# Kernel tuning notes

Hardware: AMD Instinct MI355X
Metric: run time of the kernel (lower is better)

The kernel has to match this reference:

```python
import jax, jax.numpy as jnp
import numpy as np
import math

E = 512      # embed_dim
H = 8        # num_heads
HD = E // H  # head_dim
S = 2048     # seq_len
B = 4        # batch


def setup_inputs() -> dict:
    key = jax.random.key(0)
    ks = jax.random.split(key, 8)
    std = 1.0 / math.sqrt(E)
    return {
        "query": jax.random.normal(ks[0], (S, B, E), jnp.float32),
        "key": jax.random.normal(ks[1], (S, B, E), jnp.float32),
        "value": jax.random.normal(ks[2], (S, B, E), jnp.float32),
        "relative_pos_bias": jax.random.normal(ks[3], (H, S, S), jnp.float32),
        "in_proj_weight": jax.random.normal(ks[4], (3 * E, E), jnp.float32) * std,
        "in_proj_bias": jnp.zeros((3 * E,), jnp.float32),
        "out_proj_weight": jax.random.normal(ks[5], (E, E), jnp.float32) * std,
        "out_proj_bias": jnp.zeros((E,), jnp.float32),
    }


def reference(query, key, value, relative_pos_bias,
              in_proj_weight, in_proj_bias, out_proj_weight, out_proj_bias):
    # batch_first=False: inputs are (S, B, E). Self-attn style: q,k,v all projected
    # from their respective inputs with the fused in_proj (query used for q-slice, etc.)
    wq, wk, wv = jnp.split(in_proj_weight, 3, axis=0)
    bq, bk, bv = jnp.split(in_proj_bias, 3, axis=0)
    # NOTE: original applies F.linear(q, full_in_proj) then chunks, with q==query etc.
    # Here query/key/value are distinct tensors but the torch code projects qkv from
    # the SAME tensor q (the query input). Replicate that exactly:
    qkv = query @ in_proj_weight.T + in_proj_bias          # (S, B, 3E)
    q, k, v = jnp.split(qkv, 3, axis=-1)                    # each (S, B, E)
    q = q.reshape(S, B, H, HD)
    k = k.reshape(S, B, H, HD)
    v = v.reshape(S, B, H, HD)
    scale = 1.0 / math.sqrt(HD)
    # scores: (B, H, S, S)
    scores = jnp.einsum('ibhd,jbhd->bhij', q, k) * scale
    bias = jnp.clip(relative_pos_bias, -5.0, 5.0)[None]     # (1, H, S, S)
    scores = scores + bias * 0.05
    scores = jnp.clip(scores, -30.0, 30.0)
    m = jax.lax.stop_gradient(jnp.max(scores, axis=-1, keepdims=True))
    attn_weights = jax.nn.softmax(scores - m, axis=-1)       # (B, H, S, S)
    out = jnp.einsum('bhij,jbhd->ibhd', attn_weights, v)     # (S, B, H, HD)
    out = jnp.where(jnp.isnan(out), 0.0, out)
    # torch: view(B,H,S,hd).transpose(1,2).view(B,S,E) == our (S,B,H,HD)->(B,S,E)
    out = out.transpose(1, 0, 2, 3).reshape(B, S, E)
    out = jnp.clip(out, -10.0, 10.0)
    out = out @ out_proj_weight.T + out_proj_bias            # (B, S, E)
    out = jnp.where(jnp.isnan(out), 0.0, out)
    # batch_first=False: return (S, B, E)
    return out.transpose(1, 0, 2), attn_weights
```

## Files before the change

### kernel.cpp

```cpp
#include <hip/hip_runtime.h>
#include <hip/hip_bf16.h>

#define S_LEN 2048
#define BATCH 4
#define EMB   512
#define NH    8
#define HD    64
#define SB    (S_LEN*BATCH)
#define E3    (3*EMB)
#define BH    (BATCH*NH)

typedef _Float16 f16;
typedef _Float16 f16x4 __attribute__((ext_vector_type(4)));
typedef _Float16 f16x8 __attribute__((ext_vector_type(8)));
typedef float    f32x4 __attribute__((ext_vector_type(4)));

#define LDS_FENCE() do { asm volatile("s_waitcnt lgkmcnt(0)" ::: "memory"); \
                         __builtin_amdgcn_sched_barrier(0); } while (0)

__global__ __launch_bounds__(256) void k_cast(const float* __restrict__ q,
    const float* __restrict__ wi, const float* __restrict__ wo,
    f16* __restrict__ qh, f16* __restrict__ wih, f16* __restrict__ woh)
{
    const int NQ4 = (SB*EMB)/4, NW4 = (E3*EMB)/4, NO4 = (EMB*EMB)/4;
    const int total = NQ4 + NW4 + NO4;
    for (int i = blockIdx.x * 256 + threadIdx.x; i < total; i += gridDim.x * 256) {
        const float* src; f16* dst; int j;
        if (i < NQ4)            { src = q;  dst = qh;  j = i; }
        else if (i < NQ4 + NW4) { src = wi; dst = wih; j = i - NQ4; }
        else                    { src = wo; dst = woh; j = i - NQ4 - NW4; }
        f32x4 v = *(const f32x4*)(src + (size_t)j * 4);
        f16x4 h4;
        #pragma unroll
        for (int jj = 0; jj < 4; ++jj) h4[jj] = (f16)v[jj];
        *(f16x4*)(dst + (size_t)j * 4) = h4;
    }
}

__global__ __launch_bounds__(256) void k_qkv_h(const f16* __restrict__ Ah,
    const f16* __restrict__ Bw, const float* __restrict__ bin,
    f16* __restrict__ Qh, f16* __restrict__ Kh, f16* __restrict__ Vh)
{
    __shared__ f16 As[128 * 64];
    __shared__ f16 Bs[128 * 64];
    const int tid = threadIdx.x;
    const int w = tid >> 6, l = tid & 63;
    const int g = l >> 4, li = l & 15;
    const int wm = w >> 1, wn = w & 1;
    const int row0 = blockIdx.x * 128;
    const int col0 = blockIdx.y * 128;

    const int srow = tid >> 3;
    const int sch  = tid & 7;
    const f16* ga = Ah + (size_t)(row0 + srow) * EMB + sch * 8;
    const f16* gb = Bw + (size_t)(col0 + srow) * EMB + sch * 8;

    f16x8 ra[4], rb[4];
    #pragma unroll
    for (int r = 0; r < 4; ++r) {
        ra[r] = *(const f16x8*)(ga + (size_t)r * 32 * EMB);
        rb[r] = *(const f16x8*)(gb + (size_t)r * 32 * EMB);
    }

    f32x4 acc[4][4];
    const f32x4 zero = {0.f, 0.f, 0.f, 0.f};
    #pragma unroll
    for (int m = 0; m < 4; ++m)
        #pragma unroll
        for (int n = 0; n < 4; ++n) acc[m][n] = zero;

    for (int kt = 0; kt < 8; ++kt) {
        __syncthreads();
        #pragma unroll
        for (int r = 0; r < 4; ++r) {
            const int rw = srow + 32 * r;
            const int po = rw * 64 + ((sch ^ (rw & 7)) << 3);
            *(f16x8*)&As[po] = ra[r];
            *(f16x8*)&Bs[po] = rb[r];
        }
        __syncthreads();
        if (kt < 7) {
            const int kn = (kt + 1) * 64;
            #pragma unroll
            for (int r = 0; r < 4; ++r) {
                ra[r] = *(const f16x8*)(ga + kn + (size_t)r * 32 * EMB);
                rb[r] = *(const f16x8*)(gb + kn + (size_t)r * 32 * EMB);
            }
        }
        #pragma unroll
        for (int kb = 0; kb < 2; ++kb) {
            f16x8 af[4], bf[4];
            #pragma unroll
            for (int m = 0; m < 4; ++m)
                af[m] = *(const f16x8*)&As[(wm*64 + m*16 + li) * 64 +
                                           (((kb*4 + g) ^ (li & 7)) << 3)];
            #pragma unroll
            for (int n = 0; n < 4; ++n)
                bf[n] = *(const f16x8*)&Bs[(wn*64 + n*16 + li) * 64 +
                                           (((kb*4 + g) ^ (li & 7)) << 3)];
            #pragma unroll
            for (int m = 0; m < 4; ++m)
                #pragma unroll
                for (int n = 0; n < 4; ++n)
                    acc[m][n] = __builtin_amdgcn_mfma_f32_16x16x32_f16(af[m], bf[n], acc[m][n], 0, 0, 0);
        }
    }

    #pragma unroll
    for (int n = 0; n < 4; ++n) {
        const int coln  = col0 + wn*64 + n*16 + li;
        const int which = coln >> 9;
        const int h     = (coln >> 6) & 7;
        const int d     = coln & 63;
        const float bb  = bin[coln];
        f16* base = (which == 0) ? Qh : (which == 1) ? Kh : Vh;
        #pragma unroll
        for (int m = 0; m < 4; ++m) {
            const int rbase = row0 + wm*64 + m*16 + g*4;
            const int s = rbase >> 2;
            #pragma unroll
            for (int jj = 0; jj < 4; ++jj) {
                const int bh = jj * NH + h;
                base[((size_t)bh * S_LEN + s) * HD + d] = (f16)(acc[m][n][jj] + bb);
            }
        }
    }
}

__global__ __launch_bounds__(256) void k_vt(const f16* __restrict__ Vh,
                                            f16* __restrict__ Vt)
{
    __shared__ f16 T[64 * 64];
    const int tid = threadIdx.x;
    const int l = tid & 63, w = tid >> 6;
    const int bh = blockIdx.y;
    const int s0 = blockIdx.x * 64;
    const int r8 = l >> 3;
    const int ch = l & 7;

    #pragma unroll
    for (int it = 0; it < 2; ++it) {
        const int srow = it * 32 + w * 8 + r8;
        f16x8 v = *(const f16x8*)&Vh[((size_t)bh * S_LEN + s0 + srow) * HD + ch * 8];
        #pragma unroll
        for (int i = 0; i < 8; ++i) {
            const int d = ch * 8 + i;
            T[d * 64 + (((srow >> 3) ^ (d & 7)) << 3) + (srow & 7)] = v[i];
        }
    }
    __syncthreads();
    #pragma unroll
    for (int it = 0; it < 2; ++it) {
        const int d = it * 32 + w * 8 + r8;
        f16x8 v = *(const f16x8*)&T[d * 64 + ((ch ^ (d & 7)) << 3)];
        *(f16x8*)&Vt[((size_t)bh * HD + d) * S_LEN + s0 + ch * 8] = v;
    }
}

__global__ __launch_bounds__(256, 4) void k_attn(
    const f16* __restrict__ Qh, const f16* __restrict__ Kh, const f16* __restrict__ Vt,
    const float* __restrict__ rpb, float* __restrict__ att, f16* __restrict__ ctxh)
{
    __shared__ f16   KT[64*64];
    __shared__ f16   VTs[64*64];
    __shared__ float SBm[4][16*64];
    __shared__ f16   PBm[4][16*64];

    const int tid = threadIdx.x;
    const int w  = tid >> 6, l = tid & 63;
    const int g  = l >> 4, li = l & 15;
    const int l8 = l >> 3, l7 = l & 7;
    const int bx = blockIdx.x;
    const int b  = bx & 3;
    const int rt = (bx >> 2) & 31;
    const int h  = bx >> 7;
    const int bh = b * NH + h;
    const int r0 = rt * 64 + w * 16;

    const f16* qbase = Qh + ((size_t)bh * S_LEN + r0 + li) * HD;
    const f16x8 bq0 = *(const f16x8*)(qbase + g * 8);
    const f16x8 bq1 = *(const f16x8*)(qbase + 32 + g * 8);

    const int sr0 = w * 16 + l8;
    const int sr1 = sr0 + 8;
    const int scl = (l7 ^ l8) * 8;
    const f16* kg0 = Kh + ((size_t)bh * S_LEN + sr0) * HD + scl;
    const f16* kg1 = Kh + ((size_t)bh * S_LEN + sr1) * HD + scl;
    const f16* vg0 = Vt + ((size_t)bh * HD + sr0) * S_LEN + scl;
    const f16* vg1 = Vt + ((size_t)bh * HD + sr1) * S_LEN + scl;
    const int stw0 = (w * 2 + 0) * 512 + l * 8;
    const int stw1 = (w * 2 + 1) * 512 + l * 8;

    const int fK0 = li * 64 + ((g ^ (li & 7)) << 3);
    const int fK1 = li * 64 + (((g + 4) ^ (li & 7)) << 3);

    float* SBw = &SBm[w][0];
    f16*   PBw = &PBm[w][0];
    const int sbr = l8 * 64 + ((l7 ^ l8) << 2);

    const float* bias0 = rpb + ((size_t)h * S_LEN + r0 + l8) * S_LEN + l7 * 4;
    const float* bias1 = bias0 + (size_t)8 * S_LEN;
    float* att0 = att + ((size_t)bh * S_LEN + r0 + l8) * S_LEN + l7 * 4;
    float* att1 = att0 + (size_t)8 * S_LEN;

    const f32x4 zero = {0.f, 0.f, 0.f, 0.f};

    float ls0 = 0.f, ls1 = 0.f;
    f16x8 tk0 = *(const f16x8*)kg0;
    f16x8 tk1 = *(const f16x8*)kg1;
    for (int t = 0; t < 32; ++t) {
        __syncthreads();
        *(f16x8*)&KT[stw0] = tk0;
        *(f16x8*)&KT[stw1] = tk1;
        __syncthreads();
        const int tn1 = (t < 31) ? t + 1 : 31;
        tk0 = *(const f16x8*)(kg0 + (size_t)tn1 * 4096);
        tk1 = *(const f16x8*)(kg1 + (size_t)tn1 * 4096);
        #pragma unroll
        for (int half = 0; half < 2; ++half) {
            #pragma unroll
            for (int n2 = 0; n2 < 2; ++n2) {
                const int n = half * 2 + n2;
                f16x8 a0 = *(const f16x8*)&KT[n * 1024 + fK0];
                f16x8 a1 = *(const f16x8*)&KT[n * 1024 + fK1];
                f32x4 st = __builtin_amdgcn_mfma_f32_16x16x32_f16(a0, bq0, zero, 0, 0, 0);
                st = __builtin_amdgcn_mfma_f32_16x16x32_f16(a1, bq1, st, 0, 0, 0);
                *(f32x4*)&SBw[li * 64 + ((((n * 4) + g) ^ (li & 7)) << 2)] = st;
            }
            LDS_FENCE();
            #pragma unroll
            for (int i = 0; i < 2; ++i) {
                f32x4 sc = *(const f32x4*)&SBw[sbr + i * 512 + half * 32];
                f32x4 bz = *(const f32x4*)((i ? bias1 : bias0) + t * 64 + half * 32);
                float acc = 0.f;
                #pragma unroll
                for (int jj = 0; jj < 4; ++jj) {
                    float bc = fminf(fmaxf(bz[jj], -5.f), 5.f) * 0.05f;
                    float v  = sc[jj] * 0.125f + bc;
                    v = fminf(fmaxf(v, -30.f), 30.f);
                    acc += __expf(v - 30.f);
                }
                if (i) ls1 += acc; else ls0 += acc;
            }
        }
    }
    ls0 += __shfl_xor(ls0, 1); ls0 += __shfl_xor(ls0, 2); ls0 += __shfl_xor(ls0, 4);
    ls1 += __shfl_xor(ls1, 1); ls1 += __shfl_xor(ls1, 2); ls1 += __shfl_xor(ls1, 4);
    const float inv0 = 1.0f / ls0;
    const float inv1 = 1.0f / ls1;

    f32x4 o[4] = {zero, zero, zero, zero};
    tk0 = *(const f16x8*)(kg0 + (size_t)31 * 4096);
    tk1 = *(const f16x8*)(kg1 + (size_t)31 * 4096);
    f16x8 tv0 = *(const f16x8*)(vg0 + (size_t)31 * 64);
    f16x8 tv1 = *(const f16x8*)(vg1 + (size_t)31 * 64);
    for (int tt = 0; tt < 32; ++tt) {
        const int t = 31 - tt;
        __syncthreads();
        *(f16x8*)&KT[stw0]  = tk0;
        *(f16x8*)&KT[stw1]  = tk1;
        *(f16x8*)&VTs[stw0] = tv0;
        *(f16x8*)&VTs[stw1] = tv1;
        __syncthreads();
        const int tp = (t > 0) ? t - 1 : 0;
        tk0 = *(const f16x8*)(kg0 + (size_t)tp * 4096);
        tk1 = *(const f16x8*)(kg1 + (size_t)tp * 4096);
        tv0 = *(const f16x8*)(vg0 + (size_t)tp * 64);
        tv1 = *(const f16x8*)(vg1 + (size_t)tp * 64);
        #pragma unroll
        for (int half = 0; half < 2; ++half) {
            #pragma unroll
            for (int n2 = 0; n2 < 2; ++n2) {
                const int n = half * 2 + n2;
                f16x8 a0 = *(const f16x8*)&KT[n * 1024 + fK0];
                f16x8 a1 = *(const f16x8*)&KT[n * 1024 + fK1];
                f32x4 st = __builtin_amdgcn_mfma_f32_16x16x32_f16(a0, bq0, zero, 0, 0, 0);
                st = __builtin_amdgcn_mfma_f32_16x16x32_f16(a1, bq1, st, 0, 0, 0);
                *(f32x4*)&SBw[li * 64 + ((((n * 4) + g) ^ (li & 7)) << 2)] = st;
            }
            LDS_FENCE();
            #pragma unroll
            for (int i = 0; i < 2; ++i) {
                f32x4 sc = *(const f32x4*)&SBw[sbr + i * 512 + half * 32];
                f32x4 bz = *(const f32x4*)((i ? bias1 : bias0) + t * 64 + half * 32);
                const float invi = i ? inv1 : inv0;
                f32x4 w4;
                f16x4 p4;
                #pragma unroll
                for (int jj = 0; jj < 4; ++jj) {
                    float bc = fminf(fmaxf(bz[jj], -5.f), 5.f) * 0.05f;
                    float v  = sc[jj] * 0.125f + bc;
                    v = fminf(fmaxf(v, -30.f), 30.f);
                    float wt = __expf(v - 30.f) * invi;
                    w4[jj] = wt;
                    p4[jj] = (f16)wt;
                }
                __builtin_nontemporal_store(w4,
                    (f32x4*)((i ? att1 : att0) + t * 64 + half * 32));
                *(f16x4*)&PBw[(i * 8 + l8) * 64 +
                              (((half * 4 + (l7 >> 1)) ^ l8) << 3) + ((l & 1) << 2)] = p4;
            }
        }
        LDS_FENCE();
        const f16x8 pa0 = *(const f16x8*)&PBw[fK0];
        const f16x8 pa1 = *(const f16x8*)&PBw[fK1];
        #pragma unroll
        for (int n = 0; n < 4; ++n) {
            f16x8 v0 = *(const f16x8*)&VTs[n * 1024 + fK0];
            f16x8 v1 = *(const f16x8*)&VTs[n * 1024 + fK1];
            o[n] = __builtin_amdgcn_mfma_f32_16x16x32_f16(pa0, v0, o[n], 0, 0, 0);
            o[n] = __builtin_amdgcn_mfma_f32_16x16x32_f16(pa1, v1, o[n], 0, 0, 0);
        }
    }

    #pragma unroll
    for (int n = 0; n < 4; ++n) {
        #pragma unroll
        for (int jj = 0; jj < 4; ++jj) {
            const int row = r0 + g * 4 + jj;
            float v = fminf(fmaxf(o[n][jj], -10.f), 10.f);
            ctxh[((size_t)row * BATCH + b) * EMB + h * HD + n * 16 + li] = (f16)v;
        }
    }
}

__global__ __launch_bounds__(256) void k_outproj_h(const f16* __restrict__ Ah,
    const f16* __restrict__ Bw, const float* __restrict__ bout,
    float* __restrict__ out)
{
    __shared__ f16 As[128 * 64];
    __shared__ f16 Bs[128 * 64];
    const int tid = threadIdx.x;
    const int w = tid >> 6, l = tid & 63;
    const int g = l >> 4, li = l & 15;
    const int wm = w >> 1, wn = w & 1;
    const int row0 = blockIdx.x * 128;
    const int col0 = blockIdx.y * 128;

    const int srow = tid >> 3;
    const int sch  = tid & 7;
    const f16* ga = Ah + (size_t)(row0 + srow) * EMB + sch * 8;
    const f16* gb = Bw + (size_t)(col0 + srow) * EMB + sch * 8;

    f16x8 ra[4], rb[4];
    #pragma unroll
    for (int r = 0; r < 4; ++r) {
        ra[r] = *(const f16x8*)(ga + (size_t)r * 32 * EMB);
        rb[r] = *(const f16x8*)(gb + (size_t)r * 32 * EMB);
    }

    f32x4 acc[4][4];
    const f32x4 zero = {0.f, 0.f, 0.f, 0.f};
    #pragma unroll
    for (int m = 0; m < 4; ++m)
        #pragma unroll
        for (int n = 0; n < 4; ++n) acc[m][n] = zero;

    for (int kt = 0; kt < 8; ++kt) {
        __syncthreads();
        #pragma unroll
        for (int r = 0; r < 4; ++r) {
            const int rw = srow + 32 * r;
            const int po = rw * 64 + ((sch ^ (rw & 7)) << 3);
            *(f16x8*)&As[po] = ra[r];
            *(f16x8*)&Bs[po] = rb[r];
        }
        __syncthreads();
        if (kt < 7) {
            const int kn = (kt + 1) * 64;
            #pragma unroll
            for (int r = 0; r < 4; ++r) {
                ra[r] = *(const f16x8*)(ga + kn + (size_t)r * 32 * EMB);
                rb[r] = *(const f16x8*)(gb + kn + (size_t)r * 32 * EMB);
            }
        }
        #pragma unroll
        for (int kb = 0; kb < 2; ++kb) {
            f16x8 af[4], bf[4];
            #pragma unroll
            for (int m = 0; m < 4; ++m)
                af[m] = *(const f16x8*)&As[(wm*64 + m*16 + li) * 64 +
                                           (((kb*4 + g) ^ (li & 7)) << 3)];
            #pragma unroll
            for (int n = 0; n < 4; ++n)
                bf[n] = *(const f16x8*)&Bs[(wn*64 + n*16 + li) * 64 +
                                           (((kb*4 + g) ^ (li & 7)) << 3)];
            #pragma unroll
            for (int m = 0; m < 4; ++m)
                #pragma unroll
                for (int n = 0; n < 4; ++n)
                    acc[m][n] = __builtin_amdgcn_mfma_f32_16x16x32_f16(af[m], bf[n], acc[m][n], 0, 0, 0);
        }
    }

    #pragma unroll
    for (int n = 0; n < 4; ++n) {
        const int coln = col0 + wn*64 + n*16 + li;
        const float bb = bout[coln];
        #pragma unroll
        for (int m = 0; m < 4; ++m) {
            const int rbase = row0 + wm*64 + m*16 + g*4;
            #pragma unroll
            for (int jj = 0; jj < 4; ++jj)
                out[(size_t)(rbase + jj) * EMB + coln] = acc[m][n][jj] + bb;
        }
    }
}

extern "C" void kernel_launch(void* const* d_in, const int* in_sizes, int n_in,
                              void* d_out, int out_size, void* d_ws, size_t ws_size,
                              hipStream_t stream) {
    const float* query = (const float*)d_in[0];
    const float* rpb  = (const float*)d_in[3];
    const float* Win  = (const float*)d_in[4];
    const float* bin  = (const float*)d_in[5];
    const float* Wout = (const float*)d_in[6];
    const float* bout = (const float*)d_in[7];

    float* out = (float*)d_out;
    float* att = out + (size_t)S_LEN * BATCH * EMB;

    const size_t per = (size_t)BH * S_LEN * HD;
    f16* Qh    = (f16*)d_ws;
    f16* Kh    = Qh + per;
    f16* Vt    = Kh + per;
    f16* AqCtx = Vt + per;
    f16* Winh  = AqCtx + per;
    f16* Wouth = Winh + (size_t)E3 * EMB;
    f16* Vh    = Wouth + (size_t)EMB * EMB;

    k_cast     <<<dim3(2048),            256, 0, stream>>>(query, Win, Wout, AqCtx, Winh, Wouth);
    k_qkv_h    <<<dim3(SB/128, E3/128),  256, 0, stream>>>(AqCtx, Winh, bin, Qh, Kh, Vh);
    k_vt       <<<dim3(S_LEN/64, BH),    256, 0, stream>>>(Vh, Vt);
    k_attn     <<<dim3(4 * 32 * NH),     256, 0, stream>>>(Qh, Kh, Vt, rpb, att, AqCtx);
    k_outproj_h<<<dim3(SB/128, EMB/128), 256, 0, stream>>>(AqCtx, Wouth, bout, out);
}
```

Measured before the change: 286.3 us.

## Double attention query tile to 128 rows with 512-thread blocks

The attention kernel now runs 8 waves per block, each owning 16 query rows, so a block covers 128 rows instead of 64 and the grid is halved. Each K/V tile staged in LDS is shared by twice as many query rows, which halves K/V global loads and the per-thread staging work. The cost is more LDS per block (score and probability buffers double) and fewer, larger blocks, which can lower occupancy and gives 512 blocks for the GPU's compute units.

```diff
diff --git a/kernel.cpp b/kernel.cpp
--- a/kernel.cpp
+++ b/kernel.cpp
@@ -157,14 +157,14 @@
     }
 }
 
-__global__ __launch_bounds__(256, 4) void k_attn(
+__global__ __launch_bounds__(512, 2) void k_attn(
     const f16* __restrict__ Qh, const f16* __restrict__ Kh, const f16* __restrict__ Vt,
     const float* __restrict__ rpb, float* __restrict__ att, f16* __restrict__ ctxh)
 {
     __shared__ f16   KT[64*64];
     __shared__ f16   VTs[64*64];
-    __shared__ float SBm[4][16*64];
-    __shared__ f16   PBm[4][16*64];
+    __shared__ float SBm[8][16*64];
+    __shared__ f16   PBm[8][16*64];
 
     const int tid = threadIdx.x;
     const int w  = tid >> 6, l = tid & 63;
@@ -172,24 +172,20 @@
     const int l8 = l >> 3, l7 = l & 7;
     const int bx = blockIdx.x;
     const int b  = bx & 3;
-    const int rt = (bx >> 2) & 31;
-    const int h  = bx >> 7;
+    const int rt = (bx >> 2) & 15;
+    const int h  = bx >> 6;
     const int bh = b * NH + h;
-    const int r0 = rt * 64 + w * 16;
+    const int r0 = rt * 128 + w * 16;
 
     const f16* qbase = Qh + ((size_t)bh * S_LEN + r0 + li) * HD;
     const f16x8 bq0 = *(const f16x8*)(qbase + g * 8);
     const f16x8 bq1 = *(const f16x8*)(qbase + 32 + g * 8);
 
-    const int sr0 = w * 16 + l8;
-    const int sr1 = sr0 + 8;
+    const int sr  = w * 8 + l8;
     const int scl = (l7 ^ l8) * 8;
-    const f16* kg0 = Kh + ((size_t)bh * S_LEN + sr0) * HD + scl;
-    const f16* kg1 = Kh + ((size_t)bh * S_LEN + sr1) * HD + scl;
-    const f16* vg0 = Vt + ((size_t)bh * HD + sr0) * S_LEN + scl;
-    const f16* vg1 = Vt + ((size_t)bh * HD + sr1) * S_LEN + scl;
-    const int stw0 = (w * 2 + 0) * 512 + l * 8;
-    const int stw1 = (w * 2 + 1) * 512 + l * 8;
+    const f16* kg = Kh + ((size_t)bh * S_LEN + sr) * HD + scl;
+    const f16* vg = Vt + ((size_t)bh * HD + sr) * S_LEN + scl;
+    const int stw = w * 512 + l * 8;
 
     const int fK0 = li * 64 + ((g ^ (li & 7)) << 3);
     const int fK1 = li * 64 + (((g + 4) ^ (li & 7)) << 3);
@@ -206,16 +202,13 @@
     const f32x4 zero = {0.f, 0.f, 0.f, 0.f};
 
     float ls0 = 0.f, ls1 = 0.f;
-    f16x8 tk0 = *(const f16x8*)kg0;
-    f16x8 tk1 = *(const f16x8*)kg1;
+    f16x8 tk = *(const f16x8*)kg;
     for (int t = 0; t < 32; ++t) {
         __syncthreads();
-        *(f16x8*)&KT[stw0] = tk0;
-        *(f16x8*)&KT[stw1] = tk1;
+        *(f16x8*)&KT[stw] = tk;
         __syncthreads();
         const int tn1 = (t < 31) ? t + 1 : 31;
-        tk0 = *(const f16x8*)(kg0 + (size_t)tn1 * 4096);
-        tk1 = *(const f16x8*)(kg1 + (size_t)tn1 * 4096);
+        tk = *(const f16x8*)(kg + (size_t)tn1 * 4096);
         #pragma unroll
         for (int half = 0; half < 2; ++half) {
             #pragma unroll
@@ -250,23 +243,17 @@
     const float inv1 = 1.0f / ls1;
 
     f32x4 o[4] = {zero, zero, zero, zero};
-    tk0 = *(const f16x8*)(kg0 + (size_t)31 * 4096);
-    tk1 = *(const f16x8*)(kg1 + (size_t)31 * 4096);
-    f16x8 tv0 = *(const f16x8*)(vg0 + (size_t)31 * 64);
-    f16x8 tv1 = *(const f16x8*)(vg1 + (size_t)31 * 64);
+    tk = *(const f16x8*)(kg + (size_t)31 * 4096);
+    f16x8 tv = *(const f16x8*)(vg + (size_t)31 * 64);
     for (int tt = 0; tt < 32; ++tt) {
         const int t = 31 - tt;
         __syncthreads();
-        *(f16x8*)&KT[stw0]  = tk0;
-        *(f16x8*)&KT[stw1]  = tk1;
-        *(f16x8*)&VTs[stw0] = tv0;
-        *(f16x8*)&VTs[stw1] = tv1;
+        *(f16x8*)&KT[stw]  = tk;
+        *(f16x8*)&VTs[stw] = tv;
         __syncthreads();
         const int tp = (t > 0) ? t - 1 : 0;
-        tk0 = *(const f16x8*)(kg0 + (size_t)tp * 4096);
-        tk1 = *(const f16x8*)(kg1 + (size_t)tp * 4096);
-        tv0 = *(const f16x8*)(vg0 + (size_t)tp * 64);
-        tv1 = *(const f16x8*)(vg1 + (size_t)tp * 64);
+        tk = *(const f16x8*)(kg + (size_t)tp * 4096);
+        tv = *(const f16x8*)(vg + (size_t)tp * 64);
         #pragma unroll
         for (int half = 0; half < 2; ++half) {
             #pragma unroll
@@ -432,6 +419,6 @@
     k_cast     <<<dim3(2048),            256, 0, stream>>>(query, Win, Wout, AqCtx, Winh, Wouth);
     k_qkv_h    <<<dim3(SB/128, E3/128),  256, 0, stream>>>(AqCtx, Winh, bin, Qh, Kh, Vh);
     k_vt       <<<dim3(S_LEN/64, BH),    256, 0, stream>>>(Vh, Vt);
-    k_attn     <<<dim3(4 * 32 * NH),     256, 0, stream>>>(Qh, Kh, Vt, rpb, att, AqCtx);
+    k_attn     <<<dim3(4 * 16 * NH),     512, 0, stream>>>(Qh, Kh, Vt, rpb, att, AqCtx);
     k_outproj_h<<<dim3(SB/128, EMB/128), 256, 0, stream>>>(AqCtx, Wouth, bout, out);
 }
```

Result: slower. 372.8 us (+30.2%).
